# Optimization experiments

Hardware: AMD Instinct MI355X
Metric: run time of the kernel (lower is better)

## Reference

```python
import jax, jax.numpy as jnp
import numpy as np

B = 2
C = 256          # hidden_dim / d_model
NH = 8           # attention heads
NL = 4           # feature levels
NP = 4           # sampling points per head per level
DH = C // NH
FF = 1024
NLAYERS = 6
SHAPES = [(64, 64), (32, 32), (16, 16), (8, 8)]
CIN = 256
OUT_CH = 2
IMG = 256


def setup_inputs() -> dict:
    key = jax.random.key(0)
    ks = iter(jax.random.split(key, 64))

    def nrm(shape, s=0.02):
        return jax.random.normal(next(ks), shape, jnp.float32) * s

    inp = {}
    for i, (h, w) in enumerate(SHAPES):
        inp[f"f{i}"] = jax.random.normal(next(ks), (B, CIN, h, w), jnp.float32)
    # input_proj: 1x1 conv + GroupNorm per level
    inp["proj_w"] = nrm((NL, C, CIN))
    inp["proj_b"] = jnp.zeros((NL, C), jnp.float32)
    inp["gn_w"] = jnp.ones((NL, C), jnp.float32)
    inp["gn_b"] = jnp.zeros((NL, C), jnp.float32)
    inp["level_embed"] = nrm((NL, C), 1.0)
    # 6 encoder layers (stacked params)
    inp["so_w"] = nrm((NLAYERS, NH * NL * NP * 2, C))   # sampling offsets
    inp["so_b"] = nrm((NLAYERS, NH * NL * NP * 2), 0.1)
    inp["aw_w"] = nrm((NLAYERS, NH * NL * NP, C))       # attention weights
    inp["aw_b"] = jnp.zeros((NLAYERS, NH * NL * NP), jnp.float32)
    inp["vp_w"] = nrm((NLAYERS, C, C))                   # value proj
    inp["vp_b"] = jnp.zeros((NLAYERS, C), jnp.float32)
    inp["op_w"] = nrm((NLAYERS, C, C))                   # output proj
    inp["op_b"] = jnp.zeros((NLAYERS, C), jnp.float32)
    inp["n1_w"] = jnp.ones((NLAYERS, C), jnp.float32)
    inp["n1_b"] = jnp.zeros((NLAYERS, C), jnp.float32)
    inp["l1_w"] = nrm((NLAYERS, FF, C))
    inp["l1_b"] = jnp.zeros((NLAYERS, FF), jnp.float32)
    inp["l2_w"] = nrm((NLAYERS, C, FF))
    inp["l2_b"] = jnp.zeros((NLAYERS, C), jnp.float32)
    inp["n2_w"] = jnp.ones((NLAYERS, C), jnp.float32)
    inp["n2_b"] = jnp.zeros((NLAYERS, C), jnp.float32)
    # classifier head convs
    inp["c1_w"] = nrm((64, C, 3, 3))
    inp["c1_b"] = jnp.zeros((64,), jnp.float32)
    inp["c2_w"] = nrm((OUT_CH, 64, 3, 3))
    inp["c2_b"] = jnp.zeros((OUT_CH,), jnp.float32)
    return inp


def group_norm(x, w, b, groups=32, eps=1e-5):
    Bq, Cc, H, W = x.shape
    xg = x.reshape(Bq, groups, Cc // groups, H, W)
    mu = xg.mean((2, 3, 4), keepdims=True)
    var = xg.var((2, 3, 4), keepdims=True)
    xg = (xg - mu) * jax.lax.rsqrt(var + eps)
    return xg.reshape(Bq, Cc, H, W) * w[None, :, None, None] + b[None, :, None, None]


def layer_norm(x, w, b, eps=1e-5):
    mu = x.mean(-1, keepdims=True)
    var = x.var(-1, keepdims=True)
    return (x - mu) * jax.lax.rsqrt(var + eps) * w + b


def pos_embed_sine(h, w, num_feats=C // 2):
    # PositionEmbeddingSine(normalize=True), mask all-False -> cumsum of ones
    eps = 1e-6
    scale = 2.0 * np.pi
    y = (jnp.arange(1, h + 1, dtype=jnp.float32) / (h + eps)) * scale
    x = (jnp.arange(1, w + 1, dtype=jnp.float32) / (w + eps)) * scale
    dim_t = 10000.0 ** (2.0 * (jnp.arange(num_feats) // 2).astype(jnp.float32) / num_feats)

    def enc(v):
        p = v[:, None] / dim_t  # [n, num_feats]
        return jnp.stack([jnp.sin(p[:, 0::2]), jnp.cos(p[:, 1::2])], -1).reshape(v.shape[0], num_feats)

    pe_y = enc(y)  # [h, 128]
    pe_x = enc(x)  # [w, 128]
    pos = jnp.concatenate([
        jnp.broadcast_to(pe_y[:, None, :], (h, w, num_feats)),
        jnp.broadcast_to(pe_x[None, :, :], (h, w, num_feats)),
    ], -1)  # [h, w, C], channels = (y, x)
    return pos.reshape(h * w, C)


def reference_points(shapes):
    pts = []
    for h, w in shapes:
        ry = (jnp.arange(h, dtype=jnp.float32) + 0.5) / h
        rx = (jnp.arange(w, dtype=jnp.float32) + 0.5) / w
        gy, gx = jnp.meshgrid(ry, rx, indexing='ij')
        pts.append(jnp.stack([gx, gy], -1).reshape(-1, 2))
    return jnp.concatenate(pts, 0)  # [Lq, 2] (x, y)


def bilinear_sample(v, x, y, Hl, Wl):
    # v: [B, NH, S, DH]; x, y: [B, Lq, NH, NP] pixel coords (align_corners=False, zero padding)
    x0 = jnp.floor(x); y0 = jnp.floor(y)
    fx = x - x0; fy = y - y0
    out = 0.0
    for dx, dy, wgt in ((0, 0, (1 - fx) * (1 - fy)), (1, 0, fx * (1 - fy)),
                        (0, 1, (1 - fx) * fy), (1, 1, fx * fy)):
        xi = x0 + dx; yi = y0 + dy
        valid = ((xi >= 0) & (xi < Wl) & (yi >= 0) & (yi < Hl)).astype(v.dtype)
        idx = (jnp.clip(yi, 0, Wl and Hl - 1) * Wl + jnp.clip(xi, 0, Wl - 1)).astype(jnp.int32)
        idx = (jnp.clip(yi, 0, Hl - 1) * Wl + jnp.clip(xi, 0, Wl - 1)).astype(jnp.int32)
        idxh = idx.transpose(0, 2, 1, 3).reshape(idx.shape[0], NH, -1)  # [B,NH,Lq*NP]
        g = jnp.take_along_axis(v, idxh[..., None], axis=2)             # [B,NH,Lq*NP,DH]
        w_ = (wgt * valid).transpose(0, 2, 1, 3).reshape(idx.shape[0], NH, -1, 1)
        out = out + g * w_
    return out  # [B, NH, Lq*NP, DH]


def ms_deform_attn(query, value_in, ref, starts,
                   so_w, so_b, aw_w, aw_b, vp_w, vp_b, op_w, op_b):
    Bq, Lq, _ = query.shape
    value = value_in @ vp_w.T + vp_b                                  # [B, Lin, C]
    value = value.reshape(Bq, -1, NH, DH).transpose(0, 2, 1, 3)       # [B, NH, Lin, DH]
    off = (query @ so_w.T + so_b).reshape(Bq, Lq, NH, NL, NP, 2)
    aw = (query @ aw_w.T + aw_b).reshape(Bq, Lq, NH, NL * NP)
    aw = jax.nn.softmax(aw, -1).reshape(Bq, Lq, NH, NL, NP)
    norm = jnp.array([[w, h] for (h, w) in SHAPES], jnp.float32)       # [NL, 2] (x, y)
    # sampling locations: ref (same across levels, valid_ratios=1) + normalized offsets
    loc = ref[None, :, None, None, None, :] + off / norm[None, None, None, :, None, :]
    out = jnp.zeros((Bq, NH, Lq, DH), jnp.float32)
    for l, (Hl, Wl) in enumerate(SHAPES):
        vl = jax.lax.dynamic_slice_in_dim(value, starts[l], Hl * Wl, axis=2)
        x = loc[:, :, :, l, :, 0] * Wl - 0.5
        y = loc[:, :, :, l, :, 1] * Hl - 0.5
        samp = bilinear_sample(vl, x, y, Hl, Wl).reshape(Bq, NH, Lq, NP, DH)
        out = out + jnp.einsum('bhqp,bhqpd->bhqd', aw[:, :, :, l].transpose(0, 2, 1, 3), samp)
    out = out.transpose(0, 2, 1, 3).reshape(Bq, Lq, C)
    return out @ op_w.T + op_b


def conv3x3(x, w, b):
    y = jax.lax.conv_general_dilated(x, w, (1, 1), ((1, 1), (1, 1)),
                                     dimension_numbers=('NCHW', 'OIHW', 'NCHW'))
    return y + b[None, :, None, None]


def reference(f0, f1, f2, f3, proj_w, proj_b, gn_w, gn_b, level_embed,
              so_w, so_b, aw_w, aw_b, vp_w, vp_b, op_w, op_b,
              n1_w, n1_b, l1_w, l1_b, l2_w, l2_b, n2_w, n2_b,
              c1_w, c1_b, c2_w, c2_b):
    feats = [f0, f1, f2, f3]
    srcs, poss = [], []
    for l, (h, w) in enumerate(SHAPES):
        x = jnp.einsum('oc,bchw->bohw', proj_w[l], feats[l]) + proj_b[l][None, :, None, None]
        x = group_norm(x, gn_w[l], gn_b[l])
        srcs.append(x.reshape(B, C, h * w).transpose(0, 2, 1))   # [B, HW, C]
        poss.append(pos_embed_sine(h, w) + level_embed[l])        # [HW, C]
    src = jnp.concatenate(srcs, 1)       # [B, Lq, C]
    pos = jnp.concatenate(poss, 0)       # [Lq, C]
    ref = reference_points(SHAPES)
    starts = np.cumsum([0] + [h * w for h, w in SHAPES])[:-1].tolist()
    x = src
    for i in range(NLAYERS):  # dropout=0 (eval mode)
        q = x + pos[None]
        a = ms_deform_attn(q, x, ref, starts,
                           so_w[i], so_b[i], aw_w[i], aw_b[i],
                           vp_w[i], vp_b[i], op_w[i], op_b[i])
        x = layer_norm(x + a, n1_w[i], n1_b[i])
        ff = jax.nn.relu(x @ l1_w[i].T + l1_b[i]) @ l2_w[i].T + l2_b[i]
        x = layer_norm(x + ff, n2_w[i], n2_b[i])
    h0, w0 = SHAPES[0]
    layer0 = x[:, :h0 * w0].reshape(B, h0, w0, C).transpose(0, 3, 1, 2)
    y = jax.nn.relu(conv3x3(layer0, c1_w, c1_b))
    y = conv3x3(y, c2_w, c2_b)
    return jax.image.resize(y, (B, OUT_CH, IMG, IMG), method='bilinear')
```

## Files before the change

kernel.cpp:

```cpp
#include <hip/hip_runtime.h>
#include <hip/hip_bf16.h>
#include <math.h>

#define LQ 5440
#define CDIM 256
#define BATCH 2
#define FFDIM 1024

typedef __attribute__((ext_vector_type(8))) short bf16x8;
typedef __attribute__((ext_vector_type(4))) float f32x4;

typedef __attribute__((address_space(1))) void* gas1_t;
typedef __attribute__((address_space(3))) void* las3_t;

__device__ __forceinline__ void async16(const void* g, void* l) {
  __builtin_amdgcn_global_load_lds((gas1_t)g, (las3_t)l, 16, 0, 0);
}

#define WAIT_VM4() asm volatile("s_waitcnt vmcnt(4)" ::: "memory")
#define WAIT_VM3() asm volatile("s_waitcnt vmcnt(3)" ::: "memory")
#define WAIT_VM0() asm volatile("s_waitcnt vmcnt(0)" ::: "memory")

__device__ __forceinline__ void get_chunk(int chunk, int& l, int& row0) {
  if (chunk < 64)      { l = 0; row0 = chunk * 64; }
  else if (chunk < 80) { l = 1; row0 = (chunk - 64) * 64; }
  else if (chunk < 84) { l = 2; row0 = (chunk - 80) * 64; }
  else                 { l = 3; row0 = 0; }
}

template <bool RELU, bool OUT_F32, bool OUT_B16, bool REMAP>
__global__ __launch_bounds__(256, 2) void gemm_bf16_kernel(
    const __hip_bfloat16* __restrict__ A, const __hip_bfloat16* __restrict__ Wt,
    const float* __restrict__ bias, float* __restrict__ C,
    __hip_bfloat16* __restrict__ Cb, int M, int N, int K,
    int mrows, long obase, long obstride) {
  __shared__ __hip_bfloat16 As[3][128 * 32];
  __shared__ __hip_bfloat16 Bs[3][128 * 32];
  const int tid = threadIdx.x;
  const int bm = blockIdx.y * 128, bn = blockIdx.x * 128;
  const int lane = tid & 63, wave = tid >> 6;
  const int wr = wave >> 1, wc = wave & 1;
  const int srow = tid >> 2;
  const int scol = (tid & 3) * 8;
  const int lo0 = srow * 32 + scol;
  const int lo1 = (64 + srow) * 32 + scol;
  const __hip_bfloat16* ga0 = A + (size_t)(bm + srow) * K + scol;
  const __hip_bfloat16* ga1 = A + (size_t)(bm + 64 + srow) * K + scol;
  const __hip_bfloat16* gb0 = Wt + (size_t)(bn + srow) * K + scol;
  const __hip_bfloat16* gb1 = Wt + (size_t)(bn + 64 + srow) * K + scol;

  const int nt = K >> 5;
  async16(ga0, &As[0][lo0]);
  async16(ga1, &As[0][lo1]);
  async16(gb0, &Bs[0][lo0]);
  async16(gb1, &Bs[0][lo1]);
  async16(ga0 + 32, &As[1][lo0]);
  async16(ga1 + 32, &As[1][lo1]);
  async16(gb0 + 32, &Bs[1][lo0]);
  async16(gb1 + 32, &Bs[1][lo1]);

  f32x4 acc[4][4] = {};
  const int fr = lane & 15;
  const int ksub = (lane >> 4) * 8;

  int cur = 0, nxt = 2;
  for (int t = 0; t < nt; ++t) {
    if (t == nt - 1) WAIT_VM0(); else WAIT_VM4();
    __builtin_amdgcn_s_barrier();
    asm volatile("" ::: "memory");
    bf16x8 af[4], bfv[4];
    const __hip_bfloat16* as = As[cur];
    const __hip_bfloat16* bs = Bs[cur];
#pragma unroll
    for (int mi = 0; mi < 4; ++mi)
      af[mi] = *(const bf16x8*)&as[(wr * 64 + mi * 16 + fr) * 32 + ksub];
#pragma unroll
    for (int nj = 0; nj < 4; ++nj)
      bfv[nj] = *(const bf16x8*)&bs[(wc * 64 + nj * 16 + fr) * 32 + ksub];
    if (t + 2 < nt) {
      const int ko = (t + 2) * 32;
      async16(ga0 + ko, &As[nxt][lo0]);
      async16(ga1 + ko, &As[nxt][lo1]);
      async16(gb0 + ko, &Bs[nxt][lo0]);
      async16(gb1 + ko, &Bs[nxt][lo1]);
    }
#pragma unroll
    for (int mi = 0; mi < 4; ++mi)
#pragma unroll
      for (int nj = 0; nj < 4; ++nj)
        acc[mi][nj] = __builtin_amdgcn_mfma_f32_16x16x32_bf16(af[mi], bfv[nj],
                                                              acc[mi][nj], 0, 0, 0);
    cur = (cur == 2) ? 0 : cur + 1;
    nxt = (nxt == 2) ? 0 : nxt + 1;
  }

  const int cc = lane & 15;
  const int rbase = (lane >> 4) * 4;
  float bcol[4];
#pragma unroll
  for (int nj = 0; nj < 4; ++nj) bcol[nj] = bias[bn + wc * 64 + nj * 16 + cc];
#pragma unroll
  for (int mi = 0; mi < 4; ++mi)
#pragma unroll
    for (int nj = 0; nj < 4; ++nj) {
      int col = bn + wc * 64 + nj * 16 + cc;
#pragma unroll
      for (int r = 0; r < 4; ++r) {
        int row = bm + wr * 64 + mi * 16 + rbase + r;
        float v = acc[mi][nj][r] + bcol[nj];
        if (RELU) v = fmaxf(v, 0.f);
        if (OUT_F32) {
          size_t oaddr;
          if (REMAP)
            oaddr = (size_t)obase +
                    (row < mrows ? (size_t)row * N
                                 : (size_t)obstride + (size_t)(row - mrows) * N) +
                    col;
          else
            oaddr = (size_t)row * N + col;
          C[oaddr] = v;
        }
        if (OUT_B16) Cb[(size_t)row * N + col] = __float2bfloat16(v);
      }
    }
}

__global__ __launch_bounds__(256, 2) void conv1_mfma_kernel(
    const __hip_bfloat16* __restrict__ xb, const __hip_bfloat16* __restrict__ wc1,
    const float* __restrict__ bias, const __hip_bfloat16* __restrict__ zerob,
    __hip_bfloat16* __restrict__ c1o) {
  __shared__ __hip_bfloat16 As[3][128 * 32];
  __shared__ __hip_bfloat16 Bs[3][64 * 32];
  const int tid = threadIdx.x;
  const int b = blockIdx.x >> 5;
  const int pm = (blockIdx.x & 31) * 128;
  const int lane = tid & 63, wave = tid >> 6;
  const int sr = tid >> 2;
  const int sc = (tid & 3) * 8;
  const int loA0 = sr * 32 + sc, loA1 = (64 + sr) * 32 + sc;
  f32x4 acc[2][4] = {};
  const int fr = lane & 15, ksub = (lane >> 4) * 8;

  auto stage = [&](int kt, int buf) {
    int tap = kt >> 3;
    int kk = (kt & 7) * 32;
    int dy = tap / 3 - 1, dx = tap % 3 - 1;
    int hw0 = pm + sr;
    int y0 = (hw0 >> 6) + dy, x0 = (hw0 & 63) + dx;
    bool ok0 = (y0 >= 0 && y0 < 64 && x0 >= 0 && x0 < 64);
    const __hip_bfloat16* s0 =
        xb + ((size_t)(b * LQ) + y0 * 64 + x0) * 256 + kk + sc;
    int hw1 = pm + 64 + sr;
    int y1 = (hw1 >> 6) + dy, x1 = (hw1 & 63) + dx;
    bool ok1 = (y1 >= 0 && y1 < 64 && x1 >= 0 && x1 < 64);
    const __hip_bfloat16* s1 =
        xb + ((size_t)(b * LQ) + y1 * 64 + x1) * 256 + kk + sc;
    const __hip_bfloat16* wsrc = wc1 + (size_t)sr * 2304 + tap * 256 + kk + sc;
    async16(ok0 ? s0 : zerob, &As[buf][loA0]);
    async16(ok1 ? s1 : zerob, &As[buf][loA1]);
    async16(wsrc, &Bs[buf][loA0]);
  };
  stage(0, 0);
  stage(1, 1);
  int cur = 0, nxt = 2;
  for (int kt = 0; kt < 72; ++kt) {
    if (kt == 71) WAIT_VM0(); else WAIT_VM3();
    __builtin_amdgcn_s_barrier();
    asm volatile("" ::: "memory");
    bf16x8 af[2], bfv[4];
#pragma unroll
    for (int mi = 0; mi < 2; ++mi)
      af[mi] = *(const bf16x8*)&As[cur][(wave * 32 + mi * 16 + fr) * 32 + ksub];
#pragma unroll
    for (int nj = 0; nj < 4; ++nj)
      bfv[nj] = *(const bf16x8*)&Bs[cur][(nj * 16 + fr) * 32 + ksub];
    if (kt + 2 < 72) stage(kt + 2, nxt);
#pragma unroll
    for (int mi = 0; mi < 2; ++mi)
#pragma unroll
      for (int nj = 0; nj < 4; ++nj)
        acc[mi][nj] = __builtin_amdgcn_mfma_f32_16x16x32_bf16(
            af[mi], bfv[nj], acc[mi][nj], 0, 0, 0);
    cur = (cur == 2) ? 0 : cur + 1;
    nxt = (nxt == 2) ? 0 : nxt + 1;
  }
  const int cc = lane & 15;
  const int rbase = (lane >> 4) * 4;
#pragma unroll
  for (int mi = 0; mi < 2; ++mi)
#pragma unroll
    for (int nj = 0; nj < 4; ++nj) {
      int col = nj * 16 + cc;
      float bb = bias[col];
#pragma unroll
      for (int r = 0; r < 4; ++r) {
        int row = wave * 32 + mi * 16 + rbase + r;
        float v = fmaxf(acc[mi][nj][r] + bb, 0.f);
        c1o[(size_t)(b * 4096 + pm + row) * 64 + col] = __float2bfloat16(v);
      }
    }
}

__global__ void f2b4_kernel(const float* __restrict__ in,
                            __hip_bfloat16* __restrict__ out, int n4) {
  int i = blockIdx.x * 256 + threadIdx.x;
  if (i >= n4) return;
  float4 v = ((const float4*)in)[i];
  union { ushort4 u; __hip_bfloat16 h[4]; } p;
  p.h[0] = __float2bfloat16(v.x);
  p.h[1] = __float2bfloat16(v.y);
  p.h[2] = __float2bfloat16(v.z);
  p.h[3] = __float2bfloat16(v.w);
  ((ushort4*)out)[i] = p.u;
}

__global__ void sowa_prep_kernel(const float* __restrict__ so_w,
                                 const float* __restrict__ aw_w,
                                 __hip_bfloat16* __restrict__ out) {
  int i = blockIdx.x * 256 + threadIdx.x;
  if (i >= 6 * 384 * 256) return;
  int il = i / (384 * 256);
  int rem = i - il * 384 * 256;
  int n = rem >> 8, k = rem & 255;
  float v = (n < 256) ? so_w[(size_t)il * 65536 + n * 256 + k]
                      : aw_w[(size_t)il * 32768 + (n - 256) * 256 + k];
  out[i] = __float2bfloat16(v);
}

__global__ void sowa_bias_prep_kernel(const float* __restrict__ so_b,
                                      const float* __restrict__ aw_b,
                                      float* __restrict__ out) {
  int i = blockIdx.x * 256 + threadIdx.x;
  if (i >= 6 * 384) return;
  int il = i / 384, n = i % 384;
  out[i] = (n < 256) ? so_b[il * 256 + n] : aw_b[il * 128 + n - 256];
}

__global__ void wc1_prep_kernel(const float* __restrict__ w,
                                __hip_bfloat16* __restrict__ out) {
  int i = blockIdx.x * 256 + threadIdx.x;
  if (i >= 64 * 2304) return;
  int oc = i / 2304, r = i % 2304;
  int tap = r >> 8, ic = r & 255;
  out[i] = __float2bfloat16(w[(size_t)oc * 2304 + ic * 9 + tap]);
}

__global__ __launch_bounds__(256) void transpose_f_kernel(
    const float* __restrict__ f0, const float* __restrict__ f1,
    const float* __restrict__ f2, const float* __restrict__ f3,
    __hip_bfloat16* __restrict__ ft) {
  __shared__ float tile[64][65];
  const int HWs[4] = {4096, 1024, 256, 64};
  const int STs[4] = {0, 4096, 5120, 5376};
  int chunk = blockIdx.x, c0 = blockIdx.y * 64, b = blockIdx.z;
  int l, row0;
  get_chunk(chunk, l, row0);
  const float* fin = (l == 0) ? f0 : (l == 1) ? f1 : (l == 2) ? f2 : f3;
  const int HW = HWs[l];
  int t = threadIdx.x;
  int cr = t >> 4, hc4 = (t & 15) * 4;
#pragma unroll
  for (int p = 0; p < 4; ++p) {
    int c = c0 + p * 16 + cr;
    float4 v = *(const float4*)&fin[(size_t)(b * 256 + c) * HW + row0 + hc4];
    tile[p * 16 + cr][hc4 + 0] = v.x;
    tile[p * 16 + cr][hc4 + 1] = v.y;
    tile[p * 16 + cr][hc4 + 2] = v.z;
    tile[p * 16 + cr][hc4 + 3] = v.w;
  }
  __syncthreads();
  size_t obase = (size_t)2 * STs[l] * 256 + ((size_t)b * HW + row0) * 256 + c0;
#pragma unroll
  for (int p = 0; p < 4; ++p) {
    int r = p * 16 + cr;
    union { ushort4 u; __hip_bfloat16 h[4]; } pk;
    pk.h[0] = __float2bfloat16(tile[hc4 + 0][r]);
    pk.h[1] = __float2bfloat16(tile[hc4 + 1][r]);
    pk.h[2] = __float2bfloat16(tile[hc4 + 2][r]);
    pk.h[3] = __float2bfloat16(tile[hc4 + 3][r]);
    *(ushort4*)&ft[obase + (size_t)r * 256 + hc4] = pk.u;
  }
}

__global__ __launch_bounds__(256) void gn_part_kernel(const float* __restrict__ x,
                                                      float2* __restrict__ part) {
  const int STs[4] = {0, 4096, 5120, 5376};
  int chunk = blockIdx.x, b = blockIdx.y;
  int l, row0;
  get_chunk(chunk, l, row0);
  size_t base = ((size_t)b * LQ + STs[l] + row0) * 256;
  int t = threadIdx.x;
  int col4 = t & 63, rb = t >> 6;
  float s = 0.f, ss = 0.f;
#pragma unroll 4
  for (int i = 0; i < 16; ++i) {
    int r = rb + i * 4;
    float4 v = *(const float4*)&x[base + (size_t)r * 256 + col4 * 4];
    s += v.x + v.y + v.z + v.w;
    ss += v.x * v.x + v.y * v.y + v.z * v.z + v.w * v.w;
  }
  __shared__ float sA[256], sB[256];
  sA[t] = s;
  sB[t] = ss;
  __syncthreads();
  if (t < 64) {
    s = sA[t] + sA[t + 64] + sA[t + 128] + sA[t + 192];
    ss = sB[t] + sB[t + 64] + sB[t + 128] + sB[t + 192];
    sA[t] = s;
    sB[t] = ss;
  }
  __syncthreads();
  if (t < 32)
    part[((size_t)b * 85 + chunk) * 32 + t] =
        make_float2(sA[2 * t] + sA[2 * t + 1], sB[2 * t] + sB[2 * t + 1]);
}

__global__ void gn_finalize_kernel(const float2* __restrict__ part,
                                   float2* __restrict__ stats) {
  int t = threadIdx.x;
  int b = t >> 7, rem = t & 127, l = rem >> 5, g = rem & 31;
  const int cnt_[4] = {64, 16, 4, 1};
  const int cb_[4] = {0, 64, 80, 84};
  const int HWs[4] = {4096, 1024, 256, 64};
  float s = 0.f, ss = 0.f;
  for (int i = 0; i < cnt_[l]; ++i) {
    float2 v = part[((size_t)b * 85 + cb_[l] + i) * 32 + g];
    s += v.x;
    ss += v.y;
  }
  float n = (float)(HWs[l] * 8);
  float mu = s / n;
  float var = ss / n - mu * mu;
  stats[(b * 4 + l) * 32 + g] = make_float2(mu, rsqrtf(var + 1e-5f));
}

__device__ __forceinline__ void get_level(int t, int& l, int& hw, int& Hl, int& Wl) {
  if (t < 4096)      { l = 0; hw = t;        Hl = 64; Wl = 64; }
  else if (t < 5120) { l = 1; hw = t - 4096; Hl = 32; Wl = 32; }
  else if (t < 5376) { l = 2; hw = t - 5120; Hl = 16; Wl = 16; }
  else               { l = 3; hw = t - 5376; Hl = 8;  Wl = 8;  }
}

__global__ void gn_apply_kernel(float* __restrict__ x, __hip_bfloat16* __restrict__ xb,
                                __hip_bfloat16* __restrict__ qb,
                                const float* __restrict__ pos,
                                const float2* __restrict__ stats,
                                const float* __restrict__ gw, const float* __restrict__ gb) {
  int idx = blockIdx.x * 256 + threadIdx.x;
  if (idx >= BATCH * LQ * CDIM) return;
  int c = idx & 255;
  int tok = idx >> 8;
  int b = tok / LQ, t = tok % LQ;
  int l, hw, Hl, Wl;
  get_level(t, l, hw, Hl, Wl);
  float2 st = stats[(b * 4 + l) * 32 + (c >> 3)];
  float v = (x[idx] - st.x) * st.y * gw[l * CDIM + c] + gb[l * CDIM + c];
  x[idx] = v;
  xb[idx] = __float2bfloat16(v);
  qb[idx] = __float2bfloat16(v + pos[t * 256 + c]);
}

__global__ void pos_embed_kernel(const float* __restrict__ level_embed,
                                 float* __restrict__ pos) {
  int idx = blockIdx.x * 256 + threadIdx.x;
  if (idx >= LQ * CDIM) return;
  int t = idx >> 8, c = idx & 255;
  int l, hw, Hl, Wl;
  get_level(t, l, hw, Hl, Wl);
  int y = hw / Wl, xx = hw % Wl;
  const float twopi = 6.28318530717958647692f;
  float v; int cc;
  if (c < 128) { v = (float)(y + 1) * twopi / ((float)Hl + 1e-6f); cc = c; }
  else         { v = (float)(xx + 1) * twopi / ((float)Wl + 1e-6f); cc = c - 128; }
  int k = cc >> 1;
  float dim_t = expf((float)k * (logf(10000.0f) / 64.0f));
  float p = v / dim_t;
  float e = (cc & 1) ? cosf(p) : sinf(p);
  pos[idx] = e + level_embed[l * CDIM + c];
}

__global__ void ref_kernel(float* __restrict__ ref) {
  int t = blockIdx.x * 256 + threadIdx.x;
  if (t >= LQ) return;
  int l, hw, Hl, Wl;
  get_level(t, l, hw, Hl, Wl);
  int y = hw / Wl, xx = hw % Wl;
  ref[t * 2]     = ((float)xx + 0.5f) / (float)Wl;
  ref[t * 2 + 1] = ((float)y + 0.5f) / (float)Hl;
}

__global__ __launch_bounds__(256) void deform_attn_kernel(
    const __hip_bfloat16* __restrict__ value, const float* __restrict__ comb,
    const float* __restrict__ ref, __hip_bfloat16* __restrict__ out) {
  const int Wl_[4] = {64, 32, 16, 8};
  const int st_[4] = {0, 4096, 5120, 5376};
  int gid = blockIdx.x * 32 + (threadIdx.x >> 3);
  int lane8 = threadIdx.x & 7;
  int h = gid & 7;
  int tok = gid >> 3;
  int b = tok / LQ;
  int qi = tok - b * LQ;

  const float4* awv = (const float4*)(comb + (size_t)tok * 384 + 256 + h * 16);
  float4 q0 = awv[0], q1 = awv[1], q2 = awv[2], q3 = awv[3];
  float logit[16] = {q0.x, q0.y, q0.z, q0.w, q1.x, q1.y, q1.z, q1.w,
                     q2.x, q2.y, q2.z, q2.w, q3.x, q3.y, q3.z, q3.w};
  float mx = -1e30f;
#pragma unroll
  for (int i = 0; i < 16; ++i) mx = fmaxf(mx, logit[i]);
  const float LOG2E = 1.4426950408889634f;
  float ssum = 0.f;
#pragma unroll
  for (int i = 0; i < 16; ++i) {
    logit[i] = exp2f((logit[i] - mx) * LOG2E);
    ssum += logit[i];
  }
  float inv = 1.0f / ssum;

  float rx = ref[qi * 2], ry = ref[qi * 2 + 1];
  const float4* offv = (const float4*)(comb + (size_t)tok * 384 + h * 32);
  float acc0 = 0.f, acc1 = 0.f, acc2 = 0.f, acc3 = 0.f;

#pragma unroll
  for (int l = 0; l < 4; ++l) {
    const int Wl = Wl_[l];
    const float fW = (float)Wl;
    const __hip_bfloat16* vbase =
        value + ((size_t)b * LQ + st_[l]) * CDIM + h * 32 + lane8 * 4;
    float bx = fmaf(rx, fW, -0.5f);
    float by = fmaf(ry, fW, -0.5f);
    float4 oa = offv[l * 2], ob = offv[l * 2 + 1];
    float oxs[4] = {oa.x, oa.z, ob.x, ob.z};
    float oys[4] = {oa.y, oa.w, ob.y, ob.w};
#pragma unroll
    for (int p = 0; p < 4; ++p) {
      float px = bx + oxs[p], py = by + oys[p];
      float wgt = logit[l * 4 + p] * inv;
      float fpx = floorf(px), fpy = floorf(py);
      int x0 = (int)fpx, y0 = (int)fpy;
      float fx = px - fpx, fy = py - fpy;
      float wx0 = (x0 >= 0 && x0 < Wl) ? (1.f - fx) : 0.f;
      float wx1 = (x0 >= -1 && x0 < Wl - 1) ? fx : 0.f;
      float wy0 = (y0 >= 0 && y0 < Wl) ? (wgt * (1.f - fy)) : 0.f;
      float wy1 = (y0 >= -1 && y0 < Wl - 1) ? (wgt * fy) : 0.f;
      int xc0 = min(max(x0, 0), Wl - 1);
      int xc1 = min(max(x0 + 1, 0), Wl - 1);
      int yc0 = min(max(y0, 0), Wl - 1);
      int yc1 = min(max(y0 + 1, 0), Wl - 1);
      const __hip_bfloat16* r0 = vbase + (size_t)(yc0 * Wl) * CDIM;
      const __hip_bfloat16* r1 = vbase + (size_t)(yc1 * Wl) * CDIM;
      ushort4 u00 = *(const ushort4*)(r0 + (size_t)xc0 * CDIM);
      ushort4 u01 = *(const ushort4*)(r0 + (size_t)xc1 * CDIM);
      ushort4 u10 = *(const ushort4*)(r1 + (size_t)xc0 * CDIM);
      ushort4 u11 = *(const ushort4*)(r1 + (size_t)xc1 * CDIM);
      float w00 = wy0 * wx0, w01 = wy0 * wx1, w10 = wy1 * wx0, w11 = wy1 * wx1;
      acc0 = fmaf(w00, __uint_as_float((unsigned)u00.x << 16), acc0);
      acc1 = fmaf(w00, __uint_as_float((unsigned)u00.y << 16), acc1);
      acc2 = fmaf(w00, __uint_as_float((unsigned)u00.z << 16), acc2);
      acc3 = fmaf(w00, __uint_as_float((unsigned)u00.w << 16), acc3);
      acc0 = fmaf(w01, __uint_as_float((unsigned)u01.x << 16), acc0);
      acc1 = fmaf(w01, __uint_as_float((unsigned)u01.y << 16), acc1);
      acc2 = fmaf(w01, __uint_as_float((unsigned)u01.z << 16), acc2);
      acc3 = fmaf(w01, __uint_as_float((unsigned)u01.w << 16), acc3);
      acc0 = fmaf(w10, __uint_as_float((unsigned)u10.x << 16), acc0);
      acc1 = fmaf(w10, __uint_as_float((unsigned)u10.y << 16), acc1);
      acc2 = fmaf(w10, __uint_as_float((unsigned)u10.z << 16), acc2);
      acc3 = fmaf(w10, __uint_as_float((unsigned)u10.w << 16), acc3);
      acc0 = fmaf(w11, __uint_as_float((unsigned)u11.x << 16), acc0);
      acc1 = fmaf(w11, __uint_as_float((unsigned)u11.y << 16), acc1);
      acc2 = fmaf(w11, __uint_as_float((unsigned)u11.z << 16), acc2);
      acc3 = fmaf(w11, __uint_as_float((unsigned)u11.w << 16), acc3);
    }
  }
  union { ushort4 u; __hip_bfloat16 hh[4]; } pk;
  pk.hh[0] = __float2bfloat16(acc0);
  pk.hh[1] = __float2bfloat16(acc1);
  pk.hh[2] = __float2bfloat16(acc2);
  pk.hh[3] = __float2bfloat16(acc3);
  *(ushort4*)(out + (size_t)tok * CDIM + h * 32 + lane8 * 4) = pk.u;
}

template <bool EMIT_Q>
__global__ __launch_bounds__(256) void add_ln_kernel(
    float* __restrict__ x, __hip_bfloat16* __restrict__ xb,
    __hip_bfloat16* __restrict__ qb, const float* __restrict__ pos,
    const float* __restrict__ r, const float* __restrict__ w,
    const float* __restrict__ b) {
  int wid = threadIdx.x >> 6, lane = threadIdx.x & 63;
  size_t tok = (size_t)blockIdx.x * 4 + wid;
  size_t base = tok * CDIM + lane * 4;
  float4 xv = *(const float4*)&x[base];
  float4 rv = *(const float4*)&r[base];
  float v[4] = {xv.x + rv.x, xv.y + rv.y, xv.z + rv.z, xv.w + rv.w};
  float s = v[0] + v[1] + v[2] + v[3];
  float ss = v[0] * v[0] + v[1] * v[1] + v[2] * v[2] + v[3] * v[3];
#pragma unroll
  for (int o = 1; o < 64; o <<= 1) { s += __shfl_xor(s, o); ss += __shfl_xor(ss, o); }
  float mu = s * (1.0f / 256.0f);
  float var = ss * (1.0f / 256.0f) - mu * mu;
  float rsig = rsqrtf(var + 1e-5f);
  int c = lane * 4;
  float4 wv = *(const float4*)&w[c];
  float4 bv = *(const float4*)&b[c];
  float4 o4;
  o4.x = (v[0] - mu) * rsig * wv.x + bv.x;
  o4.y = (v[1] - mu) * rsig * wv.y + bv.y;
  o4.z = (v[2] - mu) * rsig * wv.z + bv.z;
  o4.w = (v[3] - mu) * rsig * wv.w + bv.w;
  *(float4*)&x[base] = o4;
  union { ushort4 u; __hip_bfloat16 h[4]; } pk;
  pk.h[0] = __float2bfloat16(o4.x);
  pk.h[1] = __float2bfloat16(o4.y);
  pk.h[2] = __float2bfloat16(o4.z);
  pk.h[3] = __float2bfloat16(o4.w);
  *(ushort4*)&xb[base] = pk.u;
  if (EMIT_Q) {
    int t = (int)(tok >= LQ ? tok - LQ : tok);
    float4 pv = *(const float4*)&pos[(size_t)t * CDIM + c];
    union { ushort4 u; __hip_bfloat16 h[4]; } pq;
    pq.h[0] = __float2bfloat16(o4.x + pv.x);
    pq.h[1] = __float2bfloat16(o4.y + pv.y);
    pq.h[2] = __float2bfloat16(o4.z + pv.z);
    pq.h[3] = __float2bfloat16(o4.w + pv.w);
    *(ushort4*)&qb[base] = pq.u;
  }
}

__global__ __launch_bounds__(256) void conv2_part_kernel(
    const __hip_bfloat16* __restrict__ c1o, const float* __restrict__ w,
    float* __restrict__ part) {
  int pix = blockIdx.x * 256 + threadIdx.x;
  int tap = blockIdx.y, b = blockIdx.z;
  int y = pix >> 6, x = pix & 63;
  int dy = tap / 3 - 1, dx = tap % 3 - 1;
  int yy = y + dy, xx = x + dx;
  bool ok = (yy >= 0 && yy < 64 && xx >= 0 && xx < 64);
  float a0 = 0.f, a1 = 0.f;
  if (ok) {
    const __hip_bfloat16* row = c1o + (size_t)(b * 4096 + yy * 64 + xx) * 64;
#pragma unroll
    for (int ic4 = 0; ic4 < 16; ++ic4) {
      ushort4 u = *(const ushort4*)(row + ic4 * 4);
      float f0 = __uint_as_float((unsigned)u.x << 16);
      float f1 = __uint_as_float((unsigned)u.y << 16);
      float f2 = __uint_as_float((unsigned)u.z << 16);
      float f3 = __uint_as_float((unsigned)u.w << 16);
      int ic = ic4 * 4;
      a0 = fmaf(w[(ic + 0) * 9 + tap], f0, a0);
      a0 = fmaf(w[(ic + 1) * 9 + tap], f1, a0);
      a0 = fmaf(w[(ic + 2) * 9 + tap], f2, a0);
      a0 = fmaf(w[(ic + 3) * 9 + tap], f3, a0);
      a1 = fmaf(w[576 + (ic + 0) * 9 + tap], f0, a1);
      a1 = fmaf(w[576 + (ic + 1) * 9 + tap], f1, a1);
      a1 = fmaf(w[576 + (ic + 2) * 9 + tap], f2, a1);
      a1 = fmaf(w[576 + (ic + 3) * 9 + tap], f3, a1);
    }
  }
  float2 o = make_float2(a0, a1);
  *(float2*)&part[((size_t)(tap * BATCH + b) * 4096 + pix) * 2] = o;
}

__global__ void conv2_reduce_kernel(const float* __restrict__ part,
                                    const float* __restrict__ bias,
                                    float* __restrict__ out) {
  int i = blockIdx.x * 256 + threadIdx.x;
  if (i >= BATCH * 4096) return;
  int b = i >> 12, pix = i & 4095;
  float s0 = bias[0], s1 = bias[1];
#pragma unroll
  for (int tap = 0; tap < 9; ++tap) {
    float2 v = *(const float2*)&part[((size_t)(tap * BATCH + b) * 4096 + pix) * 2];
    s0 += v.x; s1 += v.y;
  }
  *(float2*)&out[(size_t)i * 2] = make_float2(s0, s1);
}

__global__ void upsample_kernel(const float* __restrict__ in, float* __restrict__ out) {
  int idx = blockIdx.x * 256 + threadIdx.x;
  if (idx >= BATCH * 2 * 256 * 256) return;
  int X = idx & 255, Y = (idx >> 8) & 255, p = idx >> 16;
  int b = p >> 1, oc = p & 1;
  float tx = ((float)X + 0.5f) * 0.25f - 0.5f;
  float ty = ((float)Y + 0.5f) * 0.25f - 0.5f;
  float fxf = floorf(tx), fyf = floorf(ty);
  int x0 = (int)fxf, y0 = (int)fyf;
  float fx = tx - fxf, fy = ty - fyf;
  int x0c = min(max(x0, 0), 63), x1c = min(max(x0 + 1, 0), 63);
  int y0c = min(max(y0, 0), 63), y1c = min(max(y0 + 1, 0), 63);
  const float* ip = in + (size_t)b * 4096 * 2 + oc;
  float v = (1.f - fy) * ((1.f - fx) * ip[(y0c * 64 + x0c) * 2] + fx * ip[(y0c * 64 + x1c) * 2]) +
            fy * ((1.f - fx) * ip[(y1c * 64 + x0c) * 2] + fx * ip[(y1c * 64 + x1c) * 2]);
  out[idx] = v;
}

extern "C" void kernel_launch(void* const* d_in, const int* in_sizes, int n_in,
                              void* d_out, int out_size, void* d_ws, size_t ws_size,
                              hipStream_t stream) {
  const float* f[4] = {(const float*)d_in[0], (const float*)d_in[1],
                       (const float*)d_in[2], (const float*)d_in[3]};
  const float* proj_w = (const float*)d_in[4];
  const float* proj_b = (const float*)d_in[5];
  const float* gn_w = (const float*)d_in[6];
  const float* gn_b = (const float*)d_in[7];
  const float* level_embed = (const float*)d_in[8];
  const float* so_w = (const float*)d_in[9];
  const float* so_b = (const float*)d_in[10];
  const float* aw_w = (const float*)d_in[11];
  const float* aw_b = (const float*)d_in[12];
  const float* vp_w = (const float*)d_in[13];
  const float* vp_b = (const float*)d_in[14];
  const float* op_w = (const float*)d_in[15];
  const float* op_b = (const float*)d_in[16];
  const float* n1_w = (const float*)d_in[17];
  const float* n1_b = (const float*)d_in[18];
  const float* l1_w = (const float*)d_in[19];
  const float* l1_b = (const float*)d_in[20];
  const float* l2_w = (const float*)d_in[21];
  const float* l2_b = (const float*)d_in[22];
  const float* n2_w = (const float*)d_in[23];
  const float* n2_b = (const float*)d_in[24];
  const float* c1_w = (const float*)d_in[25];
  const float* c1_b = (const float*)d_in[26];
  const float* c2_w = (const float*)d_in[27];
  const float* c2_b = (const float*)d_in[28];
  (void)in_sizes; (void)n_in; (void)out_size; (void)ws_size;

  float* ws = (float*)d_ws;
  const size_t TOK = (size_t)BATCH * LQ * CDIM;
  size_t o = 0;
  float* x = ws + o;     o += TOK;
  float* tmp = ws + o;   o += TOK;
  float* comb = ws + o;  o += (size_t)BATCH * LQ * 384;
  float* pos = ws + o;   o += (size_t)LQ * CDIM;
  float* refb = ws + o;  o += 11008;
  float2* stats = (float2*)(ws + o); o += 512;
  float* zerof = ws + o; o += 256;
  float* sowa_bias = ws + o; o += 2304;
  float2* gnpart = (float2*)(ws + o); o += 11008;
  __hip_bfloat16* xb = (__hip_bfloat16*)(ws + o);    o += TOK / 2;
  __hip_bfloat16* qb = (__hip_bfloat16*)(ws + o);    o += TOK / 2;
  __hip_bfloat16* valb = (__hip_bfloat16*)(ws + o);  o += TOK / 2;
  __hip_bfloat16* attnb = (__hip_bfloat16*)(ws + o); o += TOK / 2;
  __hip_bfloat16* ftb = (__hip_bfloat16*)(ws + o);   o += TOK / 2;
  __hip_bfloat16* ff1b = (__hip_bfloat16*)(ws + o);  o += (size_t)BATCH * LQ * FFDIM / 2;
  __hip_bfloat16* sowa_wb = (__hip_bfloat16*)(ws + o); o += 294912;
  __hip_bfloat16* vp_wb = (__hip_bfloat16*)(ws + o); o += 196608;
  __hip_bfloat16* op_wb = (__hip_bfloat16*)(ws + o); o += 196608;
  __hip_bfloat16* l1_wb = (__hip_bfloat16*)(ws + o); o += 786432;
  __hip_bfloat16* l2_wb = (__hip_bfloat16*)(ws + o); o += 786432;
  __hip_bfloat16* proj_wb = (__hip_bfloat16*)(ws + o); o += 131072;
  __hip_bfloat16* wc1b = (__hip_bfloat16*)(ws + o);  o += 73728;
  __hip_bfloat16* c1ob = ff1b;
  float* part2 = (float*)(ff1b + 524288);
  float* c2o = part2 + 147456;

  const int HWs[4] = {4096, 1024, 256, 64};
  const int STs[4] = {0, 4096, 5120, 5376};

  hipMemsetAsync(zerof, 0, 1024, stream);
  sowa_prep_kernel<<<(589824 + 255) / 256, 256, 0, stream>>>(so_w, aw_w, sowa_wb);
  sowa_bias_prep_kernel<<<9, 256, 0, stream>>>(so_b, aw_b, sowa_bias);
  wc1_prep_kernel<<<(147456 + 255) / 256, 256, 0, stream>>>(c1_w, wc1b);
  f2b4_kernel<<<(262144 / 4 + 255) / 256, 256, 0, stream>>>(proj_w, proj_wb, 262144 / 4);
  f2b4_kernel<<<(393216 / 4 + 255) / 256, 256, 0, stream>>>(vp_w, vp_wb, 393216 / 4);
  f2b4_kernel<<<(393216 / 4 + 255) / 256, 256, 0, stream>>>(op_w, op_wb, 393216 / 4);
  f2b4_kernel<<<(1572864 / 4 + 255) / 256, 256, 0, stream>>>(l1_w, l1_wb, 1572864 / 4);
  f2b4_kernel<<<(1572864 / 4 + 255) / 256, 256, 0, stream>>>(l2_w, l2_wb, 1572864 / 4);

  transpose_f_kernel<<<dim3(85, 4, BATCH), 256, 0, stream>>>(f[0], f[1], f[2], f[3],
                                                             ftb);
  for (int l = 0; l < 4; ++l) {
    int M2 = 2 * HWs[l];
    gemm_bf16_kernel<false, true, false, true><<<dim3(2, M2 / 128), 256, 0, stream>>>(
        ftb + (size_t)2 * STs[l] * 256, proj_wb + (size_t)l * 65536,
        proj_b + (size_t)l * 256, x, nullptr, M2, 256, 256,
        HWs[l], (long)STs[l] * 256, (long)LQ * 256);
  }
  pos_embed_kernel<<<(LQ * CDIM + 255) / 256, 256, 0, stream>>>(level_embed, pos);
  ref_kernel<<<(LQ + 255) / 256, 256, 0, stream>>>(refb);
  gn_part_kernel<<<dim3(85, BATCH), 256, 0, stream>>>(x, gnpart);
  gn_finalize_kernel<<<1, 256, 0, stream>>>(gnpart, stats);
  {
    int n = BATCH * LQ * CDIM;
    gn_apply_kernel<<<(n + 255) / 256, 256, 0, stream>>>(x, xb, qb, pos, stats,
                                                         gn_w, gn_b);
  }

  const int M = BATCH * LQ;
  for (int i = 0; i < 6; ++i) {
    const __hip_bfloat16* sowa = sowa_wb + (size_t)i * 98304;
    const __hip_bfloat16* vw = vp_wb + (size_t)i * 65536;
    const __hip_bfloat16* ow = op_wb + (size_t)i * 65536;
    const __hip_bfloat16* w1 = l1_wb + (size_t)i * 262144;
    const __hip_bfloat16* w2 = l2_wb + (size_t)i * 262144;
    const float* vb = vp_b + (size_t)i * CDIM;
    const float* ob = op_b + (size_t)i * CDIM;
    const float* b1 = l1_b + (size_t)i * FFDIM;
    const float* b2 = l2_b + (size_t)i * CDIM;

    gemm_bf16_kernel<false, false, true, false><<<dim3(2, 85), 256, 0, stream>>>(
        xb, vw, vb, nullptr, valb, M, CDIM, CDIM, 0, 0, 0);
    gemm_bf16_kernel<false, true, false, false><<<dim3(3, 85), 256, 0, stream>>>(
        qb, sowa, sowa_bias + i * 384, comb, nullptr, M, 384, CDIM, 0, 0, 0);
    deform_attn_kernel<<<BATCH * LQ * 8 / 32, 256, 0, stream>>>(valb, comb, refb,
                                                                attnb);
    gemm_bf16_kernel<false, true, false, false><<<dim3(2, 85), 256, 0, stream>>>(
        attnb, ow, ob, tmp, nullptr, M, CDIM, CDIM, 0, 0, 0);
    add_ln_kernel<false><<<M / 4, 256, 0, stream>>>(
        x, xb, nullptr, nullptr, tmp, n1_w + (size_t)i * CDIM, n1_b + (size_t)i * CDIM);
    gemm_bf16_kernel<true, false, true, false><<<dim3(8, 85), 256, 0, stream>>>(
        xb, w1, b1, nullptr, ff1b, M, FFDIM, CDIM, 0, 0, 0);
    gemm_bf16_kernel<false, true, false, false><<<dim3(2, 85), 256, 0, stream>>>(
        ff1b, w2, b2, tmp, nullptr, M, CDIM, FFDIM, 0, 0, 0);
    add_ln_kernel<true><<<M / 4, 256, 0, stream>>>(
        x, xb, qb, pos, tmp, n2_w + (size_t)i * CDIM, n2_b + (size_t)i * CDIM);
  }

  conv1_mfma_kernel<<<64, 256, 0, stream>>>(xb, wc1b, c1_b,
                                            (const __hip_bfloat16*)zerof, c1ob);
  conv2_part_kernel<<<dim3(16, 9, BATCH), 256, 0, stream>>>(c1ob, c2_w, part2);
  conv2_reduce_kernel<<<(BATCH * 4096 + 255) / 256, 256, 0, stream>>>(part2, c2_b,
                                                                      c2o);
  {
    int n = BATCH * 2 * 256 * 256;
    upsample_kernel<<<(n + 255) / 256, 256, 0, stream>>>(c2o, (float*)d_out);
  }
}
```

Measured before the change: 732.0 us.

## Fuse output-projection and FFN2 GEMMs with residual add and LayerNorm

Adds a GEMM kernel whose 64-row by 256-column tile spans the full hidden dimension, so the residual add, bias and LayerNorm (plus the bf16 query emission with positional embedding) run in the GEMM epilogue. This replaces the separate add_ln kernels and the fp32 tmp round-trip for both the attention output projection and the FFN second GEMM. Weight-conversion and bias-prep kernels are also merged into fewer launches. In exchange the grid drops to 170 blocks with a narrower M tile, which may lower occupancy and per-block efficiency, especially for the K=1024 FFN GEMM.

```diff
diff --git a/kernel.cpp b/kernel.cpp
--- a/kernel.cpp
+++ b/kernel.cpp
@@ -17,6 +17,7 @@
   __builtin_amdgcn_global_load_lds((gas1_t)g, (las3_t)l, 16, 0, 0);
 }
 
+#define WAIT_VM5() asm volatile("s_waitcnt vmcnt(5)" ::: "memory")
 #define WAIT_VM4() asm volatile("s_waitcnt vmcnt(4)" ::: "memory")
 #define WAIT_VM3() asm volatile("s_waitcnt vmcnt(3)" ::: "memory")
 #define WAIT_VM0() asm volatile("s_waitcnt vmcnt(0)" ::: "memory")
@@ -121,6 +122,132 @@
           C[oaddr] = v;
         }
         if (OUT_B16) Cb[(size_t)row * N + col] = __float2bfloat16(v);
+      }
+    }
+}
+
+template <bool EMIT_Q>
+__global__ __launch_bounds__(256, 2) void gemm_ln_kernel(
+    const __hip_bfloat16* __restrict__ A, const __hip_bfloat16* __restrict__ Wt,
+    const float* __restrict__ bias, float* __restrict__ x,
+    __hip_bfloat16* __restrict__ xb, __hip_bfloat16* __restrict__ qb,
+    const float* __restrict__ pos, const float* __restrict__ lnw,
+    const float* __restrict__ lnb, int K) {
+  __shared__ __hip_bfloat16 As[3][64 * 32];
+  __shared__ __hip_bfloat16 Bs[3][256 * 32];
+  __shared__ float sred[4][64], ssred[4][64];
+  const int tid = threadIdx.x;
+  const int bm = blockIdx.x * 64;
+  const int lane = tid & 63, wv = tid >> 6;
+  const int srow = tid >> 2;
+  const int scol = (tid & 3) * 8;
+  const int loA = srow * 32 + scol;
+  const __hip_bfloat16* ga = A + (size_t)(bm + srow) * K + scol;
+  const __hip_bfloat16* gb = Wt + (size_t)srow * K + scol;
+
+  const int nt = K >> 5;
+  auto stage = [&](int t, int buf) {
+    const int ko = t * 32;
+    async16(ga + ko, &As[buf][loA]);
+#pragma unroll
+    for (int i = 0; i < 4; ++i)
+      async16(gb + (size_t)(64 * i) * K + ko, &Bs[buf][(64 * i) * 32 + loA]);
+  };
+  stage(0, 0);
+  stage(1, 1);
+
+  f32x4 acc[4][4] = {};
+  const int fr = lane & 15;
+  const int ksub = (lane >> 4) * 8;
+
+  int cur = 0, nxt = 2;
+  for (int t = 0; t < nt; ++t) {
+    if (t == nt - 1) WAIT_VM0(); else WAIT_VM5();
+    __builtin_amdgcn_s_barrier();
+    asm volatile("" ::: "memory");
+    bf16x8 af[4], bfv[4];
+#pragma unroll
+    for (int mi = 0; mi < 4; ++mi)
+      af[mi] = *(const bf16x8*)&As[cur][(mi * 16 + fr) * 32 + ksub];
+#pragma unroll
+    for (int nj = 0; nj < 4; ++nj)
+      bfv[nj] = *(const bf16x8*)&Bs[cur][(wv * 64 + nj * 16 + fr) * 32 + ksub];
+    if (t + 2 < nt) stage(t + 2, nxt);
+#pragma unroll
+    for (int mi = 0; mi < 4; ++mi)
+#pragma unroll
+      for (int nj = 0; nj < 4; ++nj)
+        acc[mi][nj] = __builtin_amdgcn_mfma_f32_16x16x32_bf16(af[mi], bfv[nj],
+                                                              acc[mi][nj], 0, 0, 0);
+    cur = (cur == 2) ? 0 : cur + 1;
+    nxt = (nxt == 2) ? 0 : nxt + 1;
+  }
+
+  const int cc = lane & 15;
+  const int rbase = (lane >> 4) * 4;
+  float bcol[4], wcol[4], bncol[4];
+#pragma unroll
+  for (int nj = 0; nj < 4; ++nj) {
+    int col = wv * 64 + nj * 16 + cc;
+    bcol[nj] = bias[col];
+    wcol[nj] = lnw[col];
+    bncol[nj] = lnb[col];
+  }
+#pragma unroll
+  for (int mi = 0; mi < 4; ++mi)
+#pragma unroll
+    for (int r = 0; r < 4; ++r) {
+      int grow = bm + mi * 16 + rbase + r;
+#pragma unroll
+      for (int nj = 0; nj < 4; ++nj) {
+        int col = wv * 64 + nj * 16 + cc;
+        acc[mi][nj][r] += bcol[nj] + x[(size_t)grow * 256 + col];
+      }
+    }
+#pragma unroll
+  for (int mi = 0; mi < 4; ++mi)
+#pragma unroll
+    for (int r = 0; r < 4; ++r) {
+      float s = 0.f, ssq = 0.f;
+#pragma unroll
+      for (int nj = 0; nj < 4; ++nj) {
+        float v = acc[mi][nj][r];
+        s += v;
+        ssq += v * v;
+      }
+#pragma unroll
+      for (int m = 1; m < 16; m <<= 1) {
+        s += __shfl_xor(s, m);
+        ssq += __shfl_xor(ssq, m);
+      }
+      if (cc == 0) {
+        int row = mi * 16 + rbase + r;
+        sred[wv][row] = s;
+        ssred[wv][row] = ssq;
+      }
+    }
+  __syncthreads();
+#pragma unroll
+  for (int mi = 0; mi < 4; ++mi)
+#pragma unroll
+    for (int r = 0; r < 4; ++r) {
+      int row = mi * 16 + rbase + r;
+      int grow = bm + row;
+      float s = sred[0][row] + sred[1][row] + sred[2][row] + sred[3][row];
+      float ssq = ssred[0][row] + ssred[1][row] + ssred[2][row] + ssred[3][row];
+      float mu = s * (1.0f / 256.0f);
+      float var = ssq * (1.0f / 256.0f) - mu * mu;
+      float rsig = rsqrtf(var + 1e-5f);
+      int tokp = grow >= LQ ? grow - LQ : grow;
+#pragma unroll
+      for (int nj = 0; nj < 4; ++nj) {
+        int col = wv * 64 + nj * 16 + cc;
+        float xn = (acc[mi][nj][r] - mu) * rsig * wcol[nj] + bncol[nj];
+        x[(size_t)grow * 256 + col] = xn;
+        xb[(size_t)grow * 256 + col] = __float2bfloat16(xn);
+        if (EMIT_Q)
+          qb[(size_t)grow * 256 + col] =
+              __float2bfloat16(xn + pos[(size_t)tokp * 256 + col]);
       }
     }
 }
@@ -201,39 +328,50 @@
     }
 }
 
-__global__ void f2b4_kernel(const float* __restrict__ in,
-                            __hip_bfloat16* __restrict__ out, int n4) {
+__global__ void f2b_multi_kernel(const float* __restrict__ p0, const float* __restrict__ p1,
+                                 const float* __restrict__ p2, const float* __restrict__ p3,
+                                 const float* __restrict__ p4,
+                                 __hip_bfloat16* __restrict__ o0, __hip_bfloat16* __restrict__ o1,
+                                 __hip_bfloat16* __restrict__ o2, __hip_bfloat16* __restrict__ o3,
+                                 __hip_bfloat16* __restrict__ o4) {
   int i = blockIdx.x * 256 + threadIdx.x;
-  if (i >= n4) return;
-  float4 v = ((const float4*)in)[i];
+  if (i >= 1048576) return;
+  const float* in;
+  __hip_bfloat16* out;
+  int j;
+  if (i < 65536)       { in = p0; out = o0; j = i; }
+  else if (i < 163840) { in = p1; out = o1; j = i - 65536; }
+  else if (i < 262144) { in = p2; out = o2; j = i - 163840; }
+  else if (i < 655360) { in = p3; out = o3; j = i - 262144; }
+  else                 { in = p4; out = o4; j = i - 655360; }
+  float4 v = ((const float4*)in)[j];
   union { ushort4 u; __hip_bfloat16 h[4]; } p;
   p.h[0] = __float2bfloat16(v.x);
   p.h[1] = __float2bfloat16(v.y);
   p.h[2] = __float2bfloat16(v.z);
   p.h[3] = __float2bfloat16(v.w);
-  ((ushort4*)out)[i] = p.u;
+  ((ushort4*)out)[j] = p.u;
 }
 
 __global__ void sowa_prep_kernel(const float* __restrict__ so_w,
                                  const float* __restrict__ aw_w,
-                                 __hip_bfloat16* __restrict__ out) {
+                                 const float* __restrict__ so_b,
+                                 const float* __restrict__ aw_b,
+                                 __hip_bfloat16* __restrict__ out,
+                                 float* __restrict__ bias_out) {
   int i = blockIdx.x * 256 + threadIdx.x;
-  if (i >= 6 * 384 * 256) return;
-  int il = i / (384 * 256);
-  int rem = i - il * 384 * 256;
-  int n = rem >> 8, k = rem & 255;
-  float v = (n < 256) ? so_w[(size_t)il * 65536 + n * 256 + k]
-                      : aw_w[(size_t)il * 32768 + (n - 256) * 256 + k];
-  out[i] = __float2bfloat16(v);
-}
-
-__global__ void sowa_bias_prep_kernel(const float* __restrict__ so_b,
-                                      const float* __restrict__ aw_b,
-                                      float* __restrict__ out) {
-  int i = blockIdx.x * 256 + threadIdx.x;
-  if (i >= 6 * 384) return;
-  int il = i / 384, n = i % 384;
-  out[i] = (n < 256) ? so_b[il * 256 + n] : aw_b[il * 128 + n - 256];
+  if (i < 6 * 384 * 256) {
+    int il = i / (384 * 256);
+    int rem = i - il * 384 * 256;
+    int n = rem >> 8, k = rem & 255;
+    float v = (n < 256) ? so_w[(size_t)il * 65536 + n * 256 + k]
+                        : aw_w[(size_t)il * 32768 + (n - 256) * 256 + k];
+    out[i] = __float2bfloat16(v);
+  } else if (i < 6 * 384 * 256 + 6 * 384) {
+    int j = i - 6 * 384 * 256;
+    int il = j / 384, n = j % 384;
+    bias_out[j] = (n < 256) ? so_b[il * 256 + n] : aw_b[il * 128 + n - 256];
+  }
 }
 
 __global__ void wc1_prep_kernel(const float* __restrict__ w,
@@ -480,52 +618,6 @@
   *(ushort4*)(out + (size_t)tok * CDIM + h * 32 + lane8 * 4) = pk.u;
 }
 
-template <bool EMIT_Q>
-__global__ __launch_bounds__(256) void add_ln_kernel(
-    float* __restrict__ x, __hip_bfloat16* __restrict__ xb,
-    __hip_bfloat16* __restrict__ qb, const float* __restrict__ pos,
-    const float* __restrict__ r, const float* __restrict__ w,
-    const float* __restrict__ b) {
-  int wid = threadIdx.x >> 6, lane = threadIdx.x & 63;
-  size_t tok = (size_t)blockIdx.x * 4 + wid;
-  size_t base = tok * CDIM + lane * 4;
-  float4 xv = *(const float4*)&x[base];
-  float4 rv = *(const float4*)&r[base];
-  float v[4] = {xv.x + rv.x, xv.y + rv.y, xv.z + rv.z, xv.w + rv.w};
-  float s = v[0] + v[1] + v[2] + v[3];
-  float ss = v[0] * v[0] + v[1] * v[1] + v[2] * v[2] + v[3] * v[3];
-#pragma unroll
-  for (int o = 1; o < 64; o <<= 1) { s += __shfl_xor(s, o); ss += __shfl_xor(ss, o); }
-  float mu = s * (1.0f / 256.0f);
-  float var = ss * (1.0f / 256.0f) - mu * mu;
-  float rsig = rsqrtf(var + 1e-5f);
-  int c = lane * 4;
-  float4 wv = *(const float4*)&w[c];
-  float4 bv = *(const float4*)&b[c];
-  float4 o4;
-  o4.x = (v[0] - mu) * rsig * wv.x + bv.x;
-  o4.y = (v[1] - mu) * rsig * wv.y + bv.y;
-  o4.z = (v[2] - mu) * rsig * wv.z + bv.z;
-  o4.w = (v[3] - mu) * rsig * wv.w + bv.w;
-  *(float4*)&x[base] = o4;
-  union { ushort4 u; __hip_bfloat16 h[4]; } pk;
-  pk.h[0] = __float2bfloat16(o4.x);
-  pk.h[1] = __float2bfloat16(o4.y);
-  pk.h[2] = __float2bfloat16(o4.z);
-  pk.h[3] = __float2bfloat16(o4.w);
-  *(ushort4*)&xb[base] = pk.u;
-  if (EMIT_Q) {
-    int t = (int)(tok >= LQ ? tok - LQ : tok);
-    float4 pv = *(const float4*)&pos[(size_t)t * CDIM + c];
-    union { ushort4 u; __hip_bfloat16 h[4]; } pq;
-    pq.h[0] = __float2bfloat16(o4.x + pv.x);
-    pq.h[1] = __float2bfloat16(o4.y + pv.y);
-    pq.h[2] = __float2bfloat16(o4.z + pv.z);
-    pq.h[3] = __float2bfloat16(o4.w + pv.w);
-    *(ushort4*)&qb[base] = pq.u;
-  }
-}
-
 __global__ __launch_bounds__(256) void conv2_part_kernel(
     const __hip_bfloat16* __restrict__ c1o, const float* __restrict__ w,
     float* __restrict__ part) {
@@ -629,7 +721,6 @@
   const size_t TOK = (size_t)BATCH * LQ * CDIM;
   size_t o = 0;
   float* x = ws + o;     o += TOK;
-  float* tmp = ws + o;   o += TOK;
   float* comb = ws + o;  o += (size_t)BATCH * LQ * 384;
   float* pos = ws + o;   o += (size_t)LQ * CDIM;
   float* refb = ws + o;  o += 11008;
@@ -658,14 +749,11 @@
   const int STs[4] = {0, 4096, 5120, 5376};
 
   hipMemsetAsync(zerof, 0, 1024, stream);
-  sowa_prep_kernel<<<(589824 + 255) / 256, 256, 0, stream>>>(so_w, aw_w, sowa_wb);
-  sowa_bias_prep_kernel<<<9, 256, 0, stream>>>(so_b, aw_b, sowa_bias);
+  sowa_prep_kernel<<<(6 * 384 * 256 + 6 * 384 + 255) / 256, 256, 0, stream>>>(
+      so_w, aw_w, so_b, aw_b, sowa_wb, sowa_bias);
   wc1_prep_kernel<<<(147456 + 255) / 256, 256, 0, stream>>>(c1_w, wc1b);
-  f2b4_kernel<<<(262144 / 4 + 255) / 256, 256, 0, stream>>>(proj_w, proj_wb, 262144 / 4);
-  f2b4_kernel<<<(393216 / 4 + 255) / 256, 256, 0, stream>>>(vp_w, vp_wb, 393216 / 4);
-  f2b4_kernel<<<(393216 / 4 + 255) / 256, 256, 0, stream>>>(op_w, op_wb, 393216 / 4);
-  f2b4_kernel<<<(1572864 / 4 + 255) / 256, 256, 0, stream>>>(l1_w, l1_wb, 1572864 / 4);
-  f2b4_kernel<<<(1572864 / 4 + 255) / 256, 256, 0, stream>>>(l2_w, l2_wb, 1572864 / 4);
+  f2b_multi_kernel<<<(1048576 + 255) / 256, 256, 0, stream>>>(
+      proj_w, vp_w, op_w, l1_w, l2_w, proj_wb, vp_wb, op_wb, l1_wb, l2_wb);
 
   transpose_f_kernel<<<dim3(85, 4, BATCH), 256, 0, stream>>>(f[0], f[1], f[2], f[3],
                                                              ftb);
@@ -704,16 +792,14 @@
         qb, sowa, sowa_bias + i * 384, comb, nullptr, M, 384, CDIM, 0, 0, 0);
     deform_attn_kernel<<<BATCH * LQ * 8 / 32, 256, 0, stream>>>(valb, comb, refb,
                                                                 attnb);
-    gemm_bf16_kernel<false, true, false, false><<<dim3(2, 85), 256, 0, stream>>>(
-        attnb, ow, ob, tmp, nullptr, M, CDIM, CDIM, 0, 0, 0);
-    add_ln_kernel<false><<<M / 4, 256, 0, stream>>>(
-        x, xb, nullptr, nullptr, tmp, n1_w + (size_t)i * CDIM, n1_b + (size_t)i * CDIM);
+    gemm_ln_kernel<false><<<170, 256, 0, stream>>>(
+        attnb, ow, ob, x, xb, nullptr, nullptr,
+        n1_w + (size_t)i * CDIM, n1_b + (size_t)i * CDIM, CDIM);
     gemm_bf16_kernel<true, false, true, false><<<dim3(8, 85), 256, 0, stream>>>(
         xb, w1, b1, nullptr, ff1b, M, FFDIM, CDIM, 0, 0, 0);
-    gemm_bf16_kernel<false, true, false, false><<<dim3(2, 85), 256, 0, stream>>>(
-        ff1b, w2, b2, tmp, nullptr, M, CDIM, FFDIM, 0, 0, 0);
-    add_ln_kernel<true><<<M / 4, 256, 0, stream>>>(
-        x, xb, qb, pos, tmp, n2_w + (size_t)i * CDIM, n2_b + (size_t)i * CDIM);
+    gemm_ln_kernel<true><<<170, 256, 0, stream>>>(
+        ff1b, w2, b2, x, xb, qb, pos,
+        n2_w + (size_t)i * CDIM, n2_b + (size_t)i * CDIM, FFDIM);
   }
 
   conv1_mfma_kernel<<<64, 256, 0, stream>>>(xb, wc1b, c1_b,
```

Measured after the change: 715.2 us. 2.3% less time.
